# Performance work log

Measured on AMD Instinct MI355X. Metric: run time of the kernel, lower is better.

Reference implementation:

```python
import jax, jax.numpy as jnp
import numpy as np

N, M, NNZ, D = 50000, 20000, 400000, 256
ALPHA, BETA = 0.1, 0.5


def setup_inputs() -> dict:
    key = jax.random.key(0)
    ks = jax.random.split(key, 7)
    X = jax.random.normal(ks[0], (N, D), dtype=jnp.float32)
    X0 = jax.random.normal(ks[1], (N, D), dtype=jnp.float32)
    W = jax.random.normal(ks[2], (D, D), dtype=jnp.float32) / np.sqrt(D)
    degV = jax.random.uniform(ks[3], (N, 1), dtype=jnp.float32, minval=0.1, maxval=1.0)
    degE = jax.random.uniform(ks[4], (M, 1), dtype=jnp.float32, minval=0.1, maxval=1.0)
    vertex = jax.random.randint(ks[5], (NNZ,), 0, N, dtype=jnp.int32)
    edges = jax.random.randint(ks[6], (NNZ,), 0, M, dtype=jnp.int32)
    alpha = jnp.float32(ALPHA)
    beta = jnp.float32(BETA)
    return {"X": X, "X0": X0, "W": W, "degV": degV, "degE": degE,
            "vertex": vertex, "edges": edges, "alpha": alpha, "beta": beta}


def _normalize_l2(X):
    # torch: rownorm is detached -> treat scale as constant w.r.t. grad
    rownorm = jax.lax.stop_gradient(jnp.linalg.norm(X, axis=1, keepdims=True))
    scale = jnp.where(rownorm > 0, 1.0 / rownorm, 0.0)
    return X * scale


def reference(X, X0, W, degV, degE, vertex, edges, alpha, beta):
    # hop 1: gather node features to incidences, mean-aggregate into hyperedges
    Xve = X[vertex]                                               # [NNZ, D]
    sums = jax.ops.segment_sum(Xve, edges, num_segments=M)        # [M, D]
    cnts = jax.ops.segment_sum(jnp.ones((NNZ,), X.dtype), edges, num_segments=M)
    Xe = sums / jnp.maximum(cnts, 1.0)[:, None]                   # mean (first_aggregate)
    Xe = Xe * degE
    # hop 2: gather edge features back to incidences, sum-aggregate into nodes
    Xev = Xe[edges]                                               # [NNZ, D]
    Xv = jax.ops.segment_sum(Xev, vertex, num_segments=N)         # [N, D]
    Xv = Xv * degV
    Xn = _normalize_l2(Xv)                                        # use_norm=True
    Xi = (1.0 - alpha) * Xn + alpha * X0
    out = (1.0 - beta) * Xi + beta * (Xi @ W)
    return out
```

## Files before the change

### kernel.cpp

```cpp
#include <hip/hip_runtime.h>
#include <cstdint>

static constexpr int DD = 256;
static constexpr int SNB = 64;

typedef unsigned short ushort_t;
typedef __attribute__((ext_vector_type(8))) short short8v;
typedef __attribute__((ext_vector_type(4))) float f32x4;

static __device__ inline ushort_t f2bf(float f) {
  uint32_t u = __builtin_bit_cast(uint32_t, f);
  uint32_t r = (u + 0x7fffu + ((u >> 16) & 1u)) >> 16;
  return (ushort_t)r;
}
static __device__ inline float bf2f(ushort_t u) {
  return __builtin_bit_cast(float, (uint32_t)u << 16);
}
static __device__ inline void addbf8(float* a, int4 x) {
  uint32_t ux = (uint32_t)x.x, uy = (uint32_t)x.y;
  uint32_t uz = (uint32_t)x.z, uw = (uint32_t)x.w;
  a[0] += __builtin_bit_cast(float, ux << 16);
  a[1] += __builtin_bit_cast(float, ux & 0xFFFF0000u);
  a[2] += __builtin_bit_cast(float, uy << 16);
  a[3] += __builtin_bit_cast(float, uy & 0xFFFF0000u);
  a[4] += __builtin_bit_cast(float, uz << 16);
  a[5] += __builtin_bit_cast(float, uz & 0xFFFF0000u);
  a[6] += __builtin_bit_cast(float, uw << 16);
  a[7] += __builtin_bit_cast(float, uw & 0xFFFF0000u);
}


__global__ void k_count(const int* __restrict__ vertex, const int* __restrict__ edges,
                        int* __restrict__ cntV, int* __restrict__ cntE, int nnz) {
  int i = blockIdx.x * blockDim.x + threadIdx.x;
  if (i < nnz) {
    atomicAdd(&cntV[vertex[i]], 1);
    atomicAdd(&cntE[edges[i]], 1);
  }
}

__device__ inline int wave_incl_scan(int v, int lane) {
  #pragma unroll
  for (int o = 1; o < 64; o <<= 1) {
    int u = __shfl_up(v, o);
    if (lane >= o) v += u;
  }
  return v;
}

__global__ __launch_bounds__(256) void k_bsum(const int* __restrict__ cntE,
                                              const int* __restrict__ cntV,
                                              int* __restrict__ bsum, int M, int N) {
  int arr = blockIdx.x >> 6;
  int b = blockIdx.x & 63;
  const int* cnt = arr ? cntV : cntE;
  int n = arr ? N : M;
  int chunk = (((n + SNB - 1) / SNB) + 3) & ~3;
  int lo = b * chunk, hi = min(lo + chunk, n);
  int s = 0;
  for (int i = lo + (int)threadIdx.x; i < hi; i += 256) s += cnt[i];
  #pragma unroll
  for (int o = 32; o; o >>= 1) s += __shfl_down(s, o);
  __shared__ int sh[4];
  if ((threadIdx.x & 63) == 0) sh[threadIdx.x >> 6] = s;
  __syncthreads();
  if (threadIdx.x == 0) bsum[blockIdx.x] = sh[0] + sh[1] + sh[2] + sh[3];
}

__global__ __launch_bounds__(128) void k_bscan(const int* __restrict__ bsum,
                                               int* __restrict__ bpre,
                                               int* __restrict__ offsE, int* __restrict__ offsV,
                                               int M, int N) {
  int t = threadIdx.x;
  int lane = t & 63;
  int v = bsum[t];
  int inc = wave_incl_scan(v, lane);
  bpre[t] = inc - v;
  if (lane == 63) {
    if (t < 64) offsE[M] = inc;
    else        offsV[N] = inc;
  }
}

__global__ __launch_bounds__(256) void k_woffs(const int* __restrict__ cntE,
                                               const int* __restrict__ cntV,
                                               const int* __restrict__ bpre,
                                               int* __restrict__ offsE, int* __restrict__ curE,
                                               int* __restrict__ offsV, int* __restrict__ curV,
                                               int M, int N) {
  int arr = blockIdx.x >> 6;
  int b = blockIdx.x & 63;
  const int* cnt = arr ? cntV : cntE;
  int* offs = arr ? offsV : offsE;
  int* cur  = arr ? curV  : curE;
  int n = arr ? N : M;
  int chunk = (((n + SNB - 1) / SNB) + 3) & ~3;
  int lo = b * chunk, hi = min(lo + chunk, n);
  if (lo >= n) return;
  int base = bpre[blockIdx.x];

  int idx = lo + (int)threadIdx.x * 4;
  int c0 = 0, c1 = 0, c2 = 0, c3 = 0;
  if (idx + 3 < hi) {
    int4 c = *reinterpret_cast<const int4*>(cnt + idx);
    c0 = c.x; c1 = c.y; c2 = c.z; c3 = c.w;
  } else if (idx < hi) {
    c0 = cnt[idx];
    if (idx + 1 < hi) c1 = cnt[idx + 1];
    if (idx + 2 < hi) c2 = cnt[idx + 2];
  }
  int tsum = c0 + c1 + c2 + c3;
  int lane = threadIdx.x & 63, wid = threadIdx.x >> 6;
  int winc = wave_incl_scan(tsum, lane);
  __shared__ int wtot[4];
  if (lane == 63) wtot[wid] = winc;
  __syncthreads();
  int wbase = 0;
  #pragma unroll
  for (int q = 0; q < 4; ++q) wbase += (q < wid) ? wtot[q] : 0;
  int excl = base + wbase + winc - tsum;
  int o0 = excl, o1 = o0 + c0, o2 = o1 + c1, o3 = o2 + c2;
  if (idx + 3 < hi) {
    *reinterpret_cast<int4*>(offs + idx) = make_int4(o0, o1, o2, o3);
    *reinterpret_cast<int4*>(cur + idx)  = make_int4(o0, o1, o2, o3);
  } else if (idx < hi) {
    offs[idx] = o0; cur[idx] = o0;
    if (idx + 1 < hi) { offs[idx + 1] = o1; cur[idx + 1] = o1; }
    if (idx + 2 < hi) { offs[idx + 2] = o2; cur[idx + 2] = o2; }
  }
}

__global__ void k_fill(const int* __restrict__ vertex, const int* __restrict__ edges,
                       int* __restrict__ curE, int* __restrict__ curV,
                       ushort_t* __restrict__ incEv, ushort_t* __restrict__ incVe, int nnz) {
  int i = blockIdx.x * blockDim.x + threadIdx.x;
  if (i < nnz) {
    int v = vertex[i], e = edges[i];
    int pe = atomicAdd(&curE[e], 1);
    incEv[pe] = (ushort_t)v;
    int pv = atomicAdd(&curV[v], 1);
    incVe[pv] = (ushort_t)e;
  }
}


__global__ __launch_bounds__(256) void k_xcvt(const float* __restrict__ X,
                                              ushort_t* __restrict__ Xbf, int total4) {
  int i = blockIdx.x * 256 + threadIdx.x;
  if (i < total4) {
    float4 v = reinterpret_cast<const float4*>(X)[i];
    ushort4 r;
    r.x = f2bf(v.x); r.y = f2bf(v.y); r.z = f2bf(v.z); r.w = f2bf(v.w);
    reinterpret_cast<ushort4*>(Xbf)[i] = r;
  }
}


__global__ void k_hop1(const ushort_t* __restrict__ Xbf, const float* __restrict__ degE,
                       const int* __restrict__ offsE, const ushort_t* __restrict__ incEv,
                       ushort_t* __restrict__ Xe, int M, int zrow) {
  int gw = (blockIdx.x * blockDim.x + threadIdx.x) >> 6;
  int lane = threadIdx.x & 63;
  if (gw >= M) return;
  int half = lane >> 5, sub = lane & 31;
  int s = offsE[gw], t = offsE[gw + 1];
  float acc[8] = {0.f, 0.f, 0.f, 0.f, 0.f, 0.f, 0.f, 0.f};
  const ushort_t* rowbase = Xbf + sub * 8;
  for (int k = s; k < t; k += 8) {
    int4 x[4];
    #pragma unroll
    for (int p = 0; p < 4; ++p) {
      int i0 = k + 2 * p + half;
      int j = min(i0, t - 1);
      int idx = (i0 < t) ? (int)incEv[j] : zrow;
      x[p] = *reinterpret_cast<const int4*>(rowbase + (size_t)idx * DD);
    }
    #pragma unroll
    for (int p = 0; p < 4; ++p) addbf8(acc, x[p]);
  }
  #pragma unroll
  for (int j = 0; j < 8; ++j) acc[j] += __shfl_xor(acc[j], 32);
  float scale = degE[gw] / fmaxf((float)(t - s), 1.0f);
  float b0 = half ? acc[4] : acc[0];
  float b1 = half ? acc[5] : acc[1];
  float b2 = half ? acc[6] : acc[2];
  float b3 = half ? acc[7] : acc[3];
  ushort4 r;
  r.x = f2bf(b0 * scale); r.y = f2bf(b1 * scale);
  r.z = f2bf(b2 * scale); r.w = f2bf(b3 * scale);
  *reinterpret_cast<ushort4*>(Xe + (size_t)gw * DD + sub * 8 + half * 4) = r;
}


__global__ void k_hop2(const ushort_t* __restrict__ Xe, const float* __restrict__ X0,
                       const float* __restrict__ degV, const int* __restrict__ offsV,
                       const ushort_t* __restrict__ incVe, const float* __restrict__ alpha_p,
                       float* __restrict__ Xi, int N, int zrow) {
  int gw = (blockIdx.x * blockDim.x + threadIdx.x) >> 6;
  int lane = threadIdx.x & 63;
  if (gw >= N) return;
  int half = lane >> 5, sub = lane & 31;
  int s = offsV[gw], t = offsV[gw + 1];
  float acc[8] = {0.f, 0.f, 0.f, 0.f, 0.f, 0.f, 0.f, 0.f};
  const ushort_t* rowbase = Xe + sub * 8;
  for (int k = s; k < t; k += 8) {
    int4 x[4];
    #pragma unroll
    for (int p = 0; p < 4; ++p) {
      int i0 = k + 2 * p + half;
      int j = min(i0, t - 1);
      int idx = (i0 < t) ? (int)incVe[j] : zrow;
      x[p] = *reinterpret_cast<const int4*>(rowbase + (size_t)idx * DD);
    }
    #pragma unroll
    for (int p = 0; p < 4; ++p) addbf8(acc, x[p]);
  }
  #pragma unroll
  for (int j = 0; j < 8; ++j) acc[j] += __shfl_xor(acc[j], 32);
  float dv = degV[gw];
  float b0 = (half ? acc[4] : acc[0]) * dv;
  float b1 = (half ? acc[5] : acc[1]) * dv;
  float b2 = (half ? acc[6] : acc[2]) * dv;
  float b3 = (half ? acc[7] : acc[3]) * dv;
  float ss = b0 * b0 + b1 * b1 + b2 * b2 + b3 * b3;
  #pragma unroll
  for (int o = 1; o < 64; o <<= 1) ss += __shfl_xor(ss, o);
  float norm = sqrtf(ss);
  float scl = (norm > 0.f) ? (1.0f / norm) : 0.f;
  float a = alpha_p[0];
  float oma = 1.0f - a;
  int f0 = sub * 8 + half * 4;
  float4 x0 = *reinterpret_cast<const float4*>(X0 + (size_t)gw * DD + f0);
  float4 r;
  r.x = oma * (b0 * scl) + a * x0.x;
  r.y = oma * (b1 * scl) + a * x0.y;
  r.z = oma * (b2 * scl) + a * x0.z;
  r.w = oma * (b3 * scl) + a * x0.w;
  *reinterpret_cast<float4*>(Xi + (size_t)gw * DD + f0) = r;
}


__global__ __launch_bounds__(256) void k_wcvt(const float* __restrict__ W,
                                              ushort_t* __restrict__ Wt,
                                              ushort_t* __restrict__ XeZ,
                                              ushort_t* __restrict__ XbfZ) {
  int t = blockIdx.x * 256 + threadIdx.x;
  int k = t >> 8, c = t & 255;
  Wt[c * 256 + k] = f2bf(W[t]);
  if (blockIdx.x == 0) {
    int4 z = make_int4(0, 0, 0, 0);
    if (threadIdx.x < 32)       reinterpret_cast<int4*>(XeZ)[threadIdx.x] = z;
    else if (threadIdx.x < 64)  reinterpret_cast<int4*>(XbfZ)[threadIdx.x - 32] = z;
  }
}


__global__ __launch_bounds__(512, 4) void k_gemm_mfma(float* XiOut,
                                                      const ushort_t* __restrict__ Wt,
                                                      const float* __restrict__ beta_p,
                                                      int nrows) {
  __shared__ ushort_t A_lds[128][36];
  __shared__ ushort_t B_lds[256][36];
  const int tid = threadIdx.x;
  const int lane = tid & 63;
  const int wid = tid >> 6;
  const int wr = wid >> 2;
  const int wc = wid & 3;
  const int l15 = lane & 15;
  const int l4  = lane >> 4;
  const int row0 = blockIdx.x * 128;

  const int t2   = tid & 1;
  const int arow = tid >> 1;

  f32x4 acc[4][4];
  #pragma unroll
  for (int m = 0; m < 4; ++m)
    #pragma unroll
    for (int n = 0; n < 4; ++n) acc[m][n] = (f32x4){0.f, 0.f, 0.f, 0.f};

  for (int k0 = 0; k0 < 256; k0 += 32) {
    if (arow < 128) {
      int grow = row0 + arow;
      float4 v0 = make_float4(0.f, 0.f, 0.f, 0.f), v1 = v0, v2 = v0, v3 = v0;
      if (grow < nrows) {
        const float* src = XiOut + (size_t)grow * 256 + k0 + t2 * 16;
        v0 = *reinterpret_cast<const float4*>(src + 0);
        v1 = *reinterpret_cast<const float4*>(src + 4);
        v2 = *reinterpret_cast<const float4*>(src + 8);
        v3 = *reinterpret_cast<const float4*>(src + 12);
      }
      uint4 pk0, pk1;
      pk0.x = (uint32_t)f2bf(v0.x) | ((uint32_t)f2bf(v0.y) << 16);
      pk0.y = (uint32_t)f2bf(v0.z) | ((uint32_t)f2bf(v0.w) << 16);
      pk0.z = (uint32_t)f2bf(v1.x) | ((uint32_t)f2bf(v1.y) << 16);
      pk0.w = (uint32_t)f2bf(v1.z) | ((uint32_t)f2bf(v1.w) << 16);
      pk1.x = (uint32_t)f2bf(v2.x) | ((uint32_t)f2bf(v2.y) << 16);
      pk1.y = (uint32_t)f2bf(v2.z) | ((uint32_t)f2bf(v2.w) << 16);
      pk1.z = (uint32_t)f2bf(v3.x) | ((uint32_t)f2bf(v3.y) << 16);
      pk1.w = (uint32_t)f2bf(v3.z) | ((uint32_t)f2bf(v3.w) << 16);
      *reinterpret_cast<uint4*>(&A_lds[arow][t2 * 16 + 0]) = pk0;
      *reinterpret_cast<uint4*>(&A_lds[arow][t2 * 16 + 8]) = pk1;
    }
    {
      const ushort_t* src = Wt + (size_t)arow * 256 + k0 + t2 * 16;
      int4 w0 = *reinterpret_cast<const int4*>(src + 0);
      int4 w1 = *reinterpret_cast<const int4*>(src + 8);
      *reinterpret_cast<int4*>(&B_lds[arow][t2 * 16 + 0]) = w0;
      *reinterpret_cast<int4*>(&B_lds[arow][t2 * 16 + 8]) = w1;
    }
    __syncthreads();
    short8v a[4], b[4];
    #pragma unroll
    for (int m = 0; m < 4; ++m)
      a[m] = *reinterpret_cast<const short8v*>(&A_lds[wr * 64 + m * 16 + l15][l4 * 8]);
    #pragma unroll
    for (int n = 0; n < 4; ++n)
      b[n] = *reinterpret_cast<const short8v*>(&B_lds[wc * 64 + n * 16 + l15][l4 * 8]);
    #pragma unroll
    for (int m = 0; m < 4; ++m)
      #pragma unroll
      for (int n = 0; n < 4; ++n)
        acc[m][n] = __builtin_amdgcn_mfma_f32_16x16x32_bf16(a[m], b[n], acc[m][n], 0, 0, 0);
    __syncthreads();
  }

  float b = beta_p[0], ob = 1.0f - b;
  int rb0 = row0 + wr * 64;
  int cb0 = wc * 64;
  #pragma unroll
  for (int m = 0; m < 4; ++m) {
    #pragma unroll
    for (int j = 0; j < 4; ++j) {
      int r = rb0 + m * 16 + l4 * 4 + j;
      if (r < nrows) {
        #pragma unroll
        for (int n = 0; n < 4; ++n) {
          size_t idx = (size_t)r * 256 + cb0 + n * 16 + l15;
          float xi = XiOut[idx];
          XiOut[idx] = ob * xi + b * acc[m][n][j];
        }
      }
    }
  }
}


extern "C" void kernel_launch(void* const* d_in, const int* in_sizes, int n_in,
                              void* d_out, int out_size, void* d_ws, size_t ws_size,
                              hipStream_t stream) {
  const float* X     = (const float*)d_in[0];
  const float* X0    = (const float*)d_in[1];
  const float* W     = (const float*)d_in[2];
  const float* degV  = (const float*)d_in[3];
  const float* degE  = (const float*)d_in[4];
  const int*   vertex= (const int*)d_in[5];
  const int*   edges = (const int*)d_in[6];
  const float* alpha = (const float*)d_in[7];
  const float* beta  = (const float*)d_in[8];

  const int N   = in_sizes[3];
  const int M   = in_sizes[4];
  const int NNZ = in_sizes[5];

  auto r4 = [](int x) { return (x + 3) & ~3; };
  const int Mr = r4(M), Nr = r4(N);

  int* w = (int*)d_ws;
  int* cntE  = w; w += Mr;
  int* cntV  = w; w += Nr;
  int* offsE = w; w += r4(M + 1);
  int* offsV = w; w += r4(N + 1);
  int* curE  = w; w += Mr;
  int* curV  = w; w += Nr;
  int* bsum  = w; w += 128;
  int* bpre  = w; w += 128;
  ushort_t* incEv16 = (ushort_t*)w; w += (NNZ + 1) / 2;
  ushort_t* incVe16 = (ushort_t*)w; w += (NNZ + 1) / 2;
  uintptr_t p = (uintptr_t)w;
  p = (p + 15) & ~(uintptr_t)15;
  ushort_t* Wt = (ushort_t*)p;
  p += (size_t)256 * 256 * sizeof(ushort_t);
  ushort_t* Xe = (ushort_t*)p;

  float*    Xi  = (float*)d_out;
  ushort_t* Xbf = (ushort_t*)d_out;

  hipMemsetAsync(cntE, 0, (size_t)(Mr + Nr) * sizeof(int), stream);

  int nb = (NNZ + 255) / 256;
  k_wcvt <<<256, 256, 0, stream>>>(W, Wt, Xe + (size_t)M * DD, Xbf + (size_t)N * DD);
  k_xcvt <<<(N * (DD / 4) + 255) / 256, 256, 0, stream>>>(X, Xbf, N * (DD / 4));
  k_count<<<nb, 256, 0, stream>>>(vertex, edges, cntV, cntE, NNZ);
  k_bsum <<<2 * SNB, 256, 0, stream>>>(cntE, cntV, bsum, M, N);
  k_bscan<<<1, 128, 0, stream>>>(bsum, bpre, offsE, offsV, M, N);
  k_woffs<<<2 * SNB, 256, 0, stream>>>(cntE, cntV, bpre, offsE, curE, offsV, curV, M, N);
  k_fill <<<nb, 256, 0, stream>>>(vertex, edges, curE, curV, incEv16, incVe16, NNZ);

  k_hop1<<<(M + 3) / 4, 256, 0, stream>>>(Xbf, degE, offsE, incEv16, Xe, M, N);
  k_hop2<<<(N + 3) / 4, 256, 0, stream>>>(Xe, X0, degV, offsV, incVe16, alpha, Xi, N, M);
  k_gemm_mfma<<<(N + 127) / 128, 512, 0, stream>>>(Xi, Wt, beta, N);
}
```

Measured before the change: 206.6 us.

## Fuse hop2 aggregation with MFMA GEMM via LDS and merge prep kernels

```diff
diff --git a/kernel.cpp b/kernel.cpp
--- a/kernel.cpp
+++ b/kernel.cpp
@@ -30,12 +30,41 @@
 }
 
 
-__global__ void k_count(const int* __restrict__ vertex, const int* __restrict__ edges,
-                        int* __restrict__ cntV, int* __restrict__ cntE, int nnz) {
-  int i = blockIdx.x * blockDim.x + threadIdx.x;
-  if (i < nnz) {
-    atomicAdd(&cntV[vertex[i]], 1);
-    atomicAdd(&cntE[edges[i]], 1);
+__global__ __launch_bounds__(256) void k_prep(const float* __restrict__ W,
+                                              ushort_t* __restrict__ Wt,
+                                              ushort_t* __restrict__ XeZ,
+                                              ushort_t* __restrict__ XbfZ,
+                                              const float* __restrict__ X,
+                                              ushort_t* __restrict__ Xbf, int total4,
+                                              const int* __restrict__ vertex,
+                                              const int* __restrict__ edges,
+                                              int* __restrict__ cntV,
+                                              int* __restrict__ cntE, int nnz,
+                                              int xb) {
+  int b = blockIdx.x;
+  if (b < 256) {
+    int t = b * 256 + threadIdx.x;
+    int k = t >> 8, c = t & 255;
+    Wt[c * 256 + k] = f2bf(W[t]);
+    if (b == 0) {
+      int4 z = make_int4(0, 0, 0, 0);
+      if (threadIdx.x < 32)       reinterpret_cast<int4*>(XeZ)[threadIdx.x] = z;
+      else if (threadIdx.x < 64)  reinterpret_cast<int4*>(XbfZ)[threadIdx.x - 32] = z;
+    }
+  } else if (b < 256 + xb) {
+    int i = (b - 256) * 256 + threadIdx.x;
+    if (i < total4) {
+      float4 v = reinterpret_cast<const float4*>(X)[i];
+      ushort4 r;
+      r.x = f2bf(v.x); r.y = f2bf(v.y); r.z = f2bf(v.z); r.w = f2bf(v.w);
+      reinterpret_cast<ushort4*>(Xbf)[i] = r;
+    }
+  } else {
+    int i = (b - 256 - xb) * 256 + threadIdx.x;
+    if (i < nnz) {
+      atomicAdd(&cntV[vertex[i]], 1);
+      atomicAdd(&cntE[edges[i]], 1);
+    }
   }
 }
 
@@ -144,18 +173,6 @@
 }
 
 
-__global__ __launch_bounds__(256) void k_xcvt(const float* __restrict__ X,
-                                              ushort_t* __restrict__ Xbf, int total4) {
-  int i = blockIdx.x * 256 + threadIdx.x;
-  if (i < total4) {
-    float4 v = reinterpret_cast<const float4*>(X)[i];
-    ushort4 r;
-    r.x = f2bf(v.x); r.y = f2bf(v.y); r.z = f2bf(v.z); r.w = f2bf(v.w);
-    reinterpret_cast<ushort4*>(Xbf)[i] = r;
-  }
-}
-
-
 __global__ void k_hop1(const ushort_t* __restrict__ Xbf, const float* __restrict__ degE,
                        const int* __restrict__ offsE, const ushort_t* __restrict__ incEv,
                        ushort_t* __restrict__ Xe, int M, int zrow) {
@@ -192,153 +209,108 @@
 }
 
 
-__global__ void k_hop2(const ushort_t* __restrict__ Xe, const float* __restrict__ X0,
-                       const float* __restrict__ degV, const int* __restrict__ offsV,
-                       const ushort_t* __restrict__ incVe, const float* __restrict__ alpha_p,
-                       float* __restrict__ Xi, int N, int zrow) {
-  int gw = (blockIdx.x * blockDim.x + threadIdx.x) >> 6;
-  int lane = threadIdx.x & 63;
-  if (gw >= N) return;
-  int half = lane >> 5, sub = lane & 31;
-  int s = offsV[gw], t = offsV[gw + 1];
-  float acc[8] = {0.f, 0.f, 0.f, 0.f, 0.f, 0.f, 0.f, 0.f};
-  const ushort_t* rowbase = Xe + sub * 8;
-  for (int k = s; k < t; k += 8) {
-    int4 x[4];
-    #pragma unroll
-    for (int p = 0; p < 4; ++p) {
-      int i0 = k + 2 * p + half;
-      int j = min(i0, t - 1);
-      int idx = (i0 < t) ? (int)incVe[j] : zrow;
-      x[p] = *reinterpret_cast<const int4*>(rowbase + (size_t)idx * DD);
-    }
-    #pragma unroll
-    for (int p = 0; p < 4; ++p) addbf8(acc, x[p]);
-  }
-  #pragma unroll
-  for (int j = 0; j < 8; ++j) acc[j] += __shfl_xor(acc[j], 32);
-  float dv = degV[gw];
-  float b0 = (half ? acc[4] : acc[0]) * dv;
-  float b1 = (half ? acc[5] : acc[1]) * dv;
-  float b2 = (half ? acc[6] : acc[2]) * dv;
-  float b3 = (half ? acc[7] : acc[3]) * dv;
-  float ss = b0 * b0 + b1 * b1 + b2 * b2 + b3 * b3;
-  #pragma unroll
-  for (int o = 1; o < 64; o <<= 1) ss += __shfl_xor(ss, o);
-  float norm = sqrtf(ss);
-  float scl = (norm > 0.f) ? (1.0f / norm) : 0.f;
-  float a = alpha_p[0];
-  float oma = 1.0f - a;
-  int f0 = sub * 8 + half * 4;
-  float4 x0 = *reinterpret_cast<const float4*>(X0 + (size_t)gw * DD + f0);
-  float4 r;
-  r.x = oma * (b0 * scl) + a * x0.x;
-  r.y = oma * (b1 * scl) + a * x0.y;
-  r.z = oma * (b2 * scl) + a * x0.z;
-  r.w = oma * (b3 * scl) + a * x0.w;
-  *reinterpret_cast<float4*>(Xi + (size_t)gw * DD + f0) = r;
-}
-
-
-__global__ __launch_bounds__(256) void k_wcvt(const float* __restrict__ W,
-                                              ushort_t* __restrict__ Wt,
-                                              ushort_t* __restrict__ XeZ,
-                                              ushort_t* __restrict__ XbfZ) {
-  int t = blockIdx.x * 256 + threadIdx.x;
-  int k = t >> 8, c = t & 255;
-  Wt[c * 256 + k] = f2bf(W[t]);
-  if (blockIdx.x == 0) {
-    int4 z = make_int4(0, 0, 0, 0);
-    if (threadIdx.x < 32)       reinterpret_cast<int4*>(XeZ)[threadIdx.x] = z;
-    else if (threadIdx.x < 64)  reinterpret_cast<int4*>(XbfZ)[threadIdx.x - 32] = z;
-  }
-}
-
-
-__global__ __launch_bounds__(512, 4) void k_gemm_mfma(float* XiOut,
-                                                      const ushort_t* __restrict__ Wt,
-                                                      const float* __restrict__ beta_p,
-                                                      int nrows) {
-  __shared__ ushort_t A_lds[128][36];
+__global__ __launch_bounds__(512, 4) void k_hop2gemm(
+    const ushort_t* __restrict__ Xe, const float* __restrict__ X0,
+    const float* __restrict__ degV, const int* __restrict__ offsV,
+    const ushort_t* __restrict__ incVe, const float* __restrict__ alpha_p,
+    const ushort_t* __restrict__ Wt, const float* __restrict__ beta_p,
+    float* __restrict__ out, int N, int zrow) {
+  __shared__ ushort_t A_lds[64][264];
   __shared__ ushort_t B_lds[256][36];
   const int tid = threadIdx.x;
   const int lane = tid & 63;
   const int wid = tid >> 6;
-  const int wr = wid >> 2;
-  const int wc = wid & 3;
-  const int l15 = lane & 15;
-  const int l4  = lane >> 4;
-  const int row0 = blockIdx.x * 128;
-
-  const int t2   = tid & 1;
-  const int arow = tid >> 1;
-
-  f32x4 acc[4][4];
-  #pragma unroll
-  for (int m = 0; m < 4; ++m)
-    #pragma unroll
-    for (int n = 0; n < 4; ++n) acc[m][n] = (f32x4){0.f, 0.f, 0.f, 0.f};
+  const int half = lane >> 5, sub = lane & 31;
+  const int row0 = blockIdx.x * 64;
+  const float a = alpha_p[0];
+  const float oma = 1.0f - a;
+
+  #pragma unroll 1
+  for (int r = wid * 8; r < wid * 8 + 8; ++r) {
+    int gw = row0 + r;
+    int f0 = sub * 8 + half * 4;
+    if (gw >= N) {
+      *reinterpret_cast<ushort4*>(&A_lds[r][f0]) = make_ushort4(0, 0, 0, 0);
+      continue;
+    }
+    int s = offsV[gw], t = offsV[gw + 1];
+    float acc[8] = {0.f, 0.f, 0.f, 0.f, 0.f, 0.f, 0.f, 0.f};
+    const ushort_t* rowbase = Xe + sub * 8;
+    for (int k = s; k < t; k += 8) {
+      int4 x[4];
+      #pragma unroll
+      for (int p = 0; p < 4; ++p) {
+        int i0 = k + 2 * p + half;
+        int j = min(i0, t - 1);
+        int idx = (i0 < t) ? (int)incVe[j] : zrow;
+        x[p] = *reinterpret_cast<const int4*>(rowbase + (size_t)idx * DD);
+      }
+      #pragma unroll
+      for (int p = 0; p < 4; ++p) addbf8(acc, x[p]);
+    }
+    #pragma unroll
+    for (int j = 0; j < 8; ++j) acc[j] += __shfl_xor(acc[j], 32);
+    float dv = degV[gw];
+    float b0 = (half ? acc[4] : acc[0]) * dv;
+    float b1 = (half ? acc[5] : acc[1]) * dv;
+    float b2 = (half ? acc[6] : acc[2]) * dv;
+    float b3 = (half ? acc[7] : acc[3]) * dv;
+    float ss = b0 * b0 + b1 * b1 + b2 * b2 + b3 * b3;
+    #pragma unroll
+    for (int o = 1; o < 64; o <<= 1) ss += __shfl_xor(ss, o);
+    float norm = sqrtf(ss);
+    float scl = (norm > 0.f) ? (1.0f / norm) : 0.f;
+    float4 x0 = *reinterpret_cast<const float4*>(X0 + (size_t)gw * DD + f0);
+    ushort4 w;
+    w.x = f2bf(oma * (b0 * scl) + a * x0.x);
+    w.y = f2bf(oma * (b1 * scl) + a * x0.y);
+    w.z = f2bf(oma * (b2 * scl) + a * x0.z);
+    w.w = f2bf(oma * (b3 * scl) + a * x0.w);
+    *reinterpret_cast<ushort4*>(&A_lds[r][f0]) = w;
+  }
+  __syncthreads();
+
+  const int wr = wid >> 2, wc = wid & 3;
+  const int l15 = lane & 15, l4 = lane >> 4;
+  const int bcol = tid >> 1, bt2 = tid & 1;
+  f32x4 acc2[2][4];
+  #pragma unroll
+  for (int m = 0; m < 2; ++m)
+    #pragma unroll
+    for (int n = 0; n < 4; ++n) acc2[m][n] = (f32x4){0.f, 0.f, 0.f, 0.f};
 
   for (int k0 = 0; k0 < 256; k0 += 32) {
-    if (arow < 128) {
-      int grow = row0 + arow;
-      float4 v0 = make_float4(0.f, 0.f, 0.f, 0.f), v1 = v0, v2 = v0, v3 = v0;
-      if (grow < nrows) {
-        const float* src = XiOut + (size_t)grow * 256 + k0 + t2 * 16;
-        v0 = *reinterpret_cast<const float4*>(src + 0);
-        v1 = *reinterpret_cast<const float4*>(src + 4);
-        v2 = *reinterpret_cast<const float4*>(src + 8);
-        v3 = *reinterpret_cast<const float4*>(src + 12);
-      }
-      uint4 pk0, pk1;
-      pk0.x = (uint32_t)f2bf(v0.x) | ((uint32_t)f2bf(v0.y) << 16);
-      pk0.y = (uint32_t)f2bf(v0.z) | ((uint32_t)f2bf(v0.w) << 16);
-      pk0.z = (uint32_t)f2bf(v1.x) | ((uint32_t)f2bf(v1.y) << 16);
-      pk0.w = (uint32_t)f2bf(v1.z) | ((uint32_t)f2bf(v1.w) << 16);
-      pk1.x = (uint32_t)f2bf(v2.x) | ((uint32_t)f2bf(v2.y) << 16);
-      pk1.y = (uint32_t)f2bf(v2.z) | ((uint32_t)f2bf(v2.w) << 16);
-      pk1.z = (uint32_t)f2bf(v3.x) | ((uint32_t)f2bf(v3.y) << 16);
-      pk1.w = (uint32_t)f2bf(v3.z) | ((uint32_t)f2bf(v3.w) << 16);
-      *reinterpret_cast<uint4*>(&A_lds[arow][t2 * 16 + 0]) = pk0;
-      *reinterpret_cast<uint4*>(&A_lds[arow][t2 * 16 + 8]) = pk1;
-    }
-    {
-      const ushort_t* src = Wt + (size_t)arow * 256 + k0 + t2 * 16;
-      int4 w0 = *reinterpret_cast<const int4*>(src + 0);
-      int4 w1 = *reinterpret_cast<const int4*>(src + 8);
-      *reinterpret_cast<int4*>(&B_lds[arow][t2 * 16 + 0]) = w0;
-      *reinterpret_cast<int4*>(&B_lds[arow][t2 * 16 + 8]) = w1;
-    }
+    const ushort_t* src = Wt + (size_t)bcol * 256 + k0 + bt2 * 16;
+    *reinterpret_cast<int4*>(&B_lds[bcol][bt2 * 16 + 0]) = *reinterpret_cast<const int4*>(src + 0);
+    *reinterpret_cast<int4*>(&B_lds[bcol][bt2 * 16 + 8]) = *reinterpret_cast<const int4*>(src + 8);
     __syncthreads();
-    short8v a[4], b[4];
-    #pragma unroll
-    for (int m = 0; m < 4; ++m)
-      a[m] = *reinterpret_cast<const short8v*>(&A_lds[wr * 64 + m * 16 + l15][l4 * 8]);
+    short8v av[2], bv[4];
+    #pragma unroll
+    for (int m = 0; m < 2; ++m)
+      av[m] = *reinterpret_cast<const short8v*>(&A_lds[wr * 32 + m * 16 + l15][k0 + l4 * 8]);
     #pragma unroll
     for (int n = 0; n < 4; ++n)
-      b[n] = *reinterpret_cast<const short8v*>(&B_lds[wc * 64 + n * 16 + l15][l4 * 8]);
-    #pragma unroll
-    for (int m = 0; m < 4; ++m)
+      bv[n] = *reinterpret_cast<const short8v*>(&B_lds[wc * 64 + n * 16 + l15][l4 * 8]);
+    #pragma unroll
+    for (int m = 0; m < 2; ++m)
       #pragma unroll
       for (int n = 0; n < 4; ++n)
-        acc[m][n] = __builtin_amdgcn_mfma_f32_16x16x32_bf16(a[m], b[n], acc[m][n], 0, 0, 0);
+        acc2[m][n] = __builtin_amdgcn_mfma_f32_16x16x32_bf16(av[m], bv[n], acc2[m][n], 0, 0, 0);
     __syncthreads();
   }
 
-  float b = beta_p[0], ob = 1.0f - b;
-  int rb0 = row0 + wr * 64;
-  int cb0 = wc * 64;
-  #pragma unroll
-  for (int m = 0; m < 4; ++m) {
+  float bta = beta_p[0], ob = 1.0f - bta;
+  #pragma unroll
+  for (int m = 0; m < 2; ++m) {
     #pragma unroll
     for (int j = 0; j < 4; ++j) {
-      int r = rb0 + m * 16 + l4 * 4 + j;
-      if (r < nrows) {
+      int lr = wr * 32 + m * 16 + l4 * 4 + j;
+      int gr = row0 + lr;
+      if (gr < N) {
         #pragma unroll
         for (int n = 0; n < 4; ++n) {
-          size_t idx = (size_t)r * 256 + cb0 + n * 16 + l15;
-          float xi = XiOut[idx];
-          XiOut[idx] = ob * xi + b * acc[m][n][j];
+          int c = wc * 64 + n * 16 + l15;
+          out[(size_t)gr * 256 + c] = ob * bf2f(A_lds[lr][c]) + bta * acc2[m][n][j];
         }
       }
     }
@@ -383,21 +355,22 @@
   p += (size_t)256 * 256 * sizeof(ushort_t);
   ushort_t* Xe = (ushort_t*)p;
 
-  float*    Xi  = (float*)d_out;
-  ushort_t* Xbf = (ushort_t*)d_out;
+  float*    outF = (float*)d_out;
+  ushort_t* Xbf  = (ushort_t*)d_out;
 
   hipMemsetAsync(cntE, 0, (size_t)(Mr + Nr) * sizeof(int), stream);
 
   int nb = (NNZ + 255) / 256;
-  k_wcvt <<<256, 256, 0, stream>>>(W, Wt, Xe + (size_t)M * DD, Xbf + (size_t)N * DD);
-  k_xcvt <<<(N * (DD / 4) + 255) / 256, 256, 0, stream>>>(X, Xbf, N * (DD / 4));
-  k_count<<<nb, 256, 0, stream>>>(vertex, edges, cntV, cntE, NNZ);
+  int xb = (N * (DD / 4) + 255) / 256;
+  k_prep<<<256 + xb + nb, 256, 0, stream>>>(W, Wt, Xe + (size_t)M * DD,
+                                            Xbf + (size_t)N * DD, X, Xbf, N * (DD / 4),
+                                            vertex, edges, cntV, cntE, NNZ, xb);
   k_bsum <<<2 * SNB, 256, 0, stream>>>(cntE, cntV, bsum, M, N);
   k_bscan<<<1, 128, 0, stream>>>(bsum, bpre, offsE, offsV, M, N);
   k_woffs<<<2 * SNB, 256, 0, stream>>>(cntE, cntV, bpre, offsE, curE, offsV, curV, M, N);
   k_fill <<<nb, 256, 0, stream>>>(vertex, edges, curE, curV, incEv16, incVe16, NNZ);
 
   k_hop1<<<(M + 3) / 4, 256, 0, stream>>>(Xbf, degE, offsE, incEv16, Xe, M, N);
-  k_hop2<<<(N + 3) / 4, 256, 0, stream>>>(Xe, X0, degV, offsV, incVe16, alpha, Xi, N, M);
-  k_gemm_mfma<<<(N + 127) / 128, 512, 0, stream>>>(Xi, Wt, beta, N);
-}
+  k_hop2gemm<<<(N + 63) / 64, 512, 0, stream>>>(Xe, X0, degV, offsV, incVe16, alpha,
+                                                Wt, beta, outF, N, M);
+}
```

New measurement: 213.6 us. 3.4% more time.
